# Optimization experiments

Measured on AMD Instinct MI355X. Metric: run time of the kernel, lower is better.

## Reference

```python
import jax, jax.numpy as jnp
import numpy as np

B, S, D, H, E, K = 16, 2048, 768, 3072, 8, 2
CAP_FACTOR = 1.25
LN_EPS = 1e-5


def setup_inputs() -> dict:
    key = jax.random.key(0)
    ks = jax.random.split(key, 6)
    scale = 0.02
    return {
        "x": jax.random.normal(ks[0], (B, S, D), jnp.float32),
        "w_gate": jax.random.normal(ks[1], (D, E), jnp.float32) * scale,  # router (eval: no noise)
        "w1": jax.random.normal(ks[2], (E, D, H), jnp.float32) * scale,
        "b1": jnp.zeros((E, H), jnp.float32),
        "w2": jax.random.normal(ks[3], (E, H, D), jnp.float32) * scale,
        "b2": jnp.zeros((E, D), jnp.float32),
        "ln_w": jnp.ones((D,), jnp.float32),
        "ln_b": jnp.zeros((D,), jnp.float32),
    }


def reference(x, w_gate, w1, b1, w2, b2, ln_w, ln_b):
    b, s, d = x.shape
    n = b * s
    capacity = int(CAP_FACTOR * n * K / E)  # static, matches _compute_capacity
    xf = x.reshape(n, d)

    # NoisyTopKRouter in eval mode: linear gate -> top-k -> softmax over top-k logits
    logits = xf @ w_gate                                   # [N, E]
    top_logits, top_idx = jax.lax.top_k(logits, K)         # [N, K]
    routing = jax.nn.softmax(top_logits, axis=-1)          # [N, K]

    out = jnp.zeros((n, d), x.dtype)
    for e in range(E):
        # per-token weight for expert e (0 if not routed to e)
        w_e = jnp.sum(routing * (top_idx == e), axis=-1)   # [N]
        # capacity dropping: keep the `capacity` highest-weight tokens.
        # Unassigned tokens have weight 0 -> zero contribution, so selecting
        # them as filler is mathematically identical to the torch loop.
        top_w, tok = jax.lax.top_k(w_e, capacity)          # [cap], [cap]
        sel = xf[tok]                                      # gather [cap, D]
        h = jax.nn.gelu(sel @ w1[e] + b1[e], approximate=False)
        y = h @ w2[e] + b2[e]                              # [cap, D]
        out = out.at[tok].add(y * top_w[:, None])          # weighted scatter-add

    out = out.reshape(b, s, d)
    mu = jnp.mean(out, axis=-1, keepdims=True)
    var = jnp.mean(jnp.square(out - mu), axis=-1, keepdims=True)
    return (out - mu) * jax.lax.rsqrt(var + LN_EPS) * ln_w + ln_b
```

## Files before the change

### kernel.cpp

```cpp
#include <hip/hip_runtime.h>
#include <math.h>

#define NTOK 32768
#define DDIM 768
#define HDIM 3072
#define NEXP 8
#define CAP  10240
#define NBLK 128

typedef short short8 __attribute__((ext_vector_type(8)));
typedef float f32x4 __attribute__((ext_vector_type(4)));

__device__ __forceinline__ unsigned short f2bf(float f) {
  unsigned u = __float_as_uint(f);
  u += 0x7FFFu + ((u >> 16) & 1u);
  return (unsigned short)(u >> 16);
}
__device__ __forceinline__ float bf2f(unsigned short h) {
  return __uint_as_float((unsigned)h << 16);
}

__device__ __forceinline__ void gload16(const void* g, void* l) {
  __builtin_amdgcn_global_load_lds(
      (const __attribute__((address_space(1))) void*)g,
      (__attribute__((address_space(3))) void*)l, 16, 0, 0);
}

__device__ __forceinline__ float gelu_fast(float v) {
  float z = v * 0.70710678118654752f;
  float a = fabsf(z);
  float t = 1.0f / (1.0f + 0.3275911f * a);
  float p = t * (0.254829592f +
           t * (-0.284496736f +
           t * (1.421413741f +
           t * (-1.453152027f +
           t * 1.061405429f))));
  float ex = __expf(-a * a);
  float er = 1.0f - p * ex;
  er = copysignf(er, z);
  return 0.5f * v * (1.0f + er);
}

__global__ __launch_bounds__(256) void router_assign(
    const float* __restrict__ x, const float* __restrict__ wg,
    unsigned short* __restrict__ xb,
    unsigned int* __restrict__ pair, float* __restrict__ pw)
{
  __shared__ float wt[NEXP][DDIM];
  int t = threadIdx.x;
  for (int idx = t; idx < NEXP * DDIM; idx += 256) {
    int d = idx >> 3, e = idx & 7;
    wt[e][d] = wg[idx];
  }
  __syncthreads();
  int wave = t >> 6, lane = t & 63;
  int n0 = blockIdx.x * 32 + wave * 8;
  for (int i = 0; i < 8; ++i) {
    int n = n0 + i;
    const float* xr = x + (size_t)n * DDIM;
    unsigned short* xbr = xb + (size_t)n * DDIM;
    float acc[NEXP];
#pragma unroll
    for (int e = 0; e < NEXP; ++e) acc[e] = 0.f;
#pragma unroll
    for (int c = 0; c < 3; ++c) {
      int d = c * 256 + lane * 4;
      float4 xv = *(const float4*)(xr + d);
      ushort4 pk;
      pk.x = f2bf(xv.x); pk.y = f2bf(xv.y); pk.z = f2bf(xv.z); pk.w = f2bf(xv.w);
      *(ushort4*)(xbr + d) = pk;
#pragma unroll
      for (int e = 0; e < NEXP; ++e) {
        float4 wv = *(const float4*)(&wt[e][d]);
        acc[e] += xv.x * wv.x + xv.y * wv.y + xv.z * wv.z + xv.w * wv.w;
      }
    }
#pragma unroll
    for (int e = 0; e < NEXP; ++e) {
      float v = acc[e];
      for (int o = 32; o > 0; o >>= 1) v += __shfl_xor(v, o, 64);
      acc[e] = v;
    }
    if (lane == 0) {
      int e1 = 0; float l1 = acc[0];
#pragma unroll
      for (int e = 1; e < NEXP; ++e) if (acc[e] > l1) { l1 = acc[e]; e1 = e; }
      int e2 = -1; float l2 = -INFINITY;
#pragma unroll
      for (int e = 0; e < NEXP; ++e) if (e != e1 && acc[e] > l2) { l2 = acc[e]; e2 = e; }
      float p1 = 1.f / (1.f + expf(l2 - l1));
      pair[n] = (unsigned)e1 | ((unsigned)e2 << 8);
      pw[n] = p1;
    }
  }
}

__global__ __launch_bounds__(256) void moe_count(
    const unsigned int* __restrict__ pair, int* __restrict__ bcnt)
{
  __shared__ int c8[NEXP];
  int b = blockIdx.x, t = threadIdx.x, lane = t & 63;
  if (t < NEXP) c8[t] = 0;
  __syncthreads();
  unsigned p = pair[b * 256 + t];
  int e1 = p & 255, e2 = (p >> 8) & 255;
#pragma unroll
  for (int e = 0; e < NEXP; ++e) {
    int c = __popcll(__ballot(e1 == e)) + __popcll(__ballot(e2 == e));
    if (lane == 0 && c) atomicAdd(&c8[e], c);
  }
  __syncthreads();
  if (t < NEXP) bcnt[b * NEXP + t] = c8[t];
}

__global__ __launch_bounds__(512) void moe_scan(
    const int* __restrict__ bcnt, int* __restrict__ bbase, int* __restrict__ cnt)
{
  int t = threadIdx.x, w = t >> 6, lane = t & 63;
  if (lane == 0) {
    int run = 0;
    for (int b = 0; b < NBLK; ++b) { bbase[b * NEXP + w] = run; run += bcnt[b * NEXP + w]; }
    cnt[w] = (run < CAP) ? run : CAP;
  }
}

__global__ __launch_bounds__(256) void moe_scatter(
    const unsigned int* __restrict__ pair, const int* __restrict__ bbase,
    int* __restrict__ tokidx, int* __restrict__ slotof)
{
  __shared__ int wcnt[4][NEXP];
  __shared__ int woffs[4][NEXP];
  int b = blockIdx.x, t = threadIdx.x, wave = t >> 6, lane = t & 63;
  int n = b * 256 + t;
  unsigned p = pair[n];
  int e1 = p & 255, e2 = (p >> 8) & 255;
  unsigned long long below = (lane == 63) ? 0x7FFFFFFFFFFFFFFFull
                                          : ((1ull << lane) - 1ull);
  int pre1 = 0, pre2 = 0;
#pragma unroll
  for (int e = 0; e < NEXP; ++e) {
    unsigned long long b1 = __ballot(e1 == e);
    unsigned long long b2 = __ballot(e2 == e);
    if (e1 == e) pre1 = __popcll(b1 & below);
    if (e2 == e) pre2 = __popcll(b1) + __popcll(b2 & below);
    if (lane == 0) wcnt[wave][e] = __popcll(b1) + __popcll(b2);
  }
  __syncthreads();
  if (t < 4 * NEXP) {
    int w = t >> 3, e = t & 7;
    int s = 0;
    for (int w2 = 0; w2 < w; ++w2) s += wcnt[w2][e];
    woffs[w][e] = s;
  }
  __syncthreads();
  int g1 = bbase[b * NEXP + e1] + woffs[wave][e1] + pre1;
  int g2 = bbase[b * NEXP + e2] + woffs[wave][e2] + pre2;
  if (g1 < CAP) { tokidx[e1 * CAP + g1] = n; slotof[2 * n] = e1 * CAP + g1; }
  else slotof[2 * n] = -1;
  if (g2 < CAP) { tokidx[e2 * CAP + g2] = n; slotof[2 * n + 1] = e2 * CAP + g2; }
  else slotof[2 * n + 1] = -1;
}

__global__ __launch_bounds__(256) void transpose_all(
    const float* __restrict__ w1, const float* __restrict__ w2,
    unsigned short* __restrict__ d1, unsigned short* __restrict__ d2)
{
  __shared__ float tile[64][65];
  int bid = blockIdx.x;
  int half = bid / (576 * NEXP);
  int r = bid - half * 576 * NEXP;
  int e = r / 576, rr = r - e * 576;
  const float* src; unsigned short* dst; int R, C, cx, cy;
  if (half == 0) { src = w1; dst = d1; R = DDIM; C = HDIM; cx = rr % 48; cy = rr / 48; }
  else           { src = w2; dst = d2; R = HDIM; C = DDIM; cx = rr % 12; cy = rr / 12; }
  const float* s = src + (size_t)e * R * C;
  unsigned short* d = dst + (size_t)e * R * C;
  int c0 = cx * 64, r0 = cy * 64;
  int tc = threadIdx.x & 63, tg = threadIdx.x >> 6;
#pragma unroll
  for (int q = tg; q < 64; q += 4)
    tile[q][tc] = s[(size_t)(r0 + q) * C + c0 + tc];
  __syncthreads();
#pragma unroll
  for (int q = tg; q < 64; q += 4)
    d[(size_t)(c0 + q) * R + r0 + tc] = f2bf(tile[tc][q]);
}

template<int EPI, int KK, int NN>
__global__ __launch_bounds__(512, 2) void moe_gemm(
    const unsigned short* __restrict__ A,
    const unsigned short* __restrict__ Bt,
    const float* __restrict__ bias,
    const int* __restrict__ cnt,
    const int* __restrict__ tokidx,
    unsigned short* __restrict__ Obuf,
    int mbase, int Mc, int mt)
{
  constexpr int KT = KK / 64;
  constexpr int NI = KT / 2;
  constexpr int GX = NN / 256;

  int nwg = gridDim.x;
  int orig = blockIdx.x;
  int q = nwg >> 3, r = nwg & 7;
  int xcd = orig & 7, loc = orig >> 3;
  int base = (xcd < r) ? xcd * (q + 1) : r * (q + 1) + (xcd - r) * q;
  int wg = base + loc;
  int per_e = GX * mt;
  int e = wg / per_e;
  int rem = wg - e * per_e;
  int by = rem / GX;
  int bx = rem - by * GX;

  int M = cnt[e]; if (M > CAP) M = CAP;
  int ly0 = by * 256;
  int gm0 = mbase + ly0;
  if (gm0 >= M) return;
  int n0 = bx * 256;
  int t = threadIdx.x, wave = t >> 6, lane = t & 63;
  int wr = wave >> 2, wc = wave & 3;
  int lane15 = lane & 15, quad = lane >> 4;

  __shared__ __align__(16) char smem[131072];

  int ci0 = wave * 128 + lane;
  int ci1 = ci0 + 64;
  int r0 = ci0 >> 2, r1 = ci1 >> 2;
  int c0 = (ci0 & 3) ^ ((r0 >> 1) & 3);
  int c1 = (ci1 & 3) ^ ((r1 >> 1) & 3);
  const unsigned short *aB0, *aB1, *bB0, *bB1;
  if (EPI == 0) {
    int g0 = gm0 + r0; if (g0 >= M) g0 = M - 1;
    int g1 = gm0 + r1; if (g1 >= M) g1 = M - 1;
    aB0 = A + (size_t)tokidx[e * CAP + g0] * KK + c0 * 8;
    aB1 = A + (size_t)tokidx[e * CAP + g1] * KK + c1 * 8;
  } else {
    aB0 = A + ((size_t)e * Mc + ly0 + r0) * KK + c0 * 8;
    aB1 = A + ((size_t)e * Mc + ly0 + r1) * KK + c1 * 8;
  }
  bB0 = Bt + ((size_t)e * NN + n0 + r0) * KK + c0 * 8;
  bB1 = Bt + ((size_t)e * NN + n0 + r1) * KK + c1 * 8;

#define STAGE_A(buf, kh, kt_) do { \
    gload16(aB0 + (kt_) * 64 + (kh) * 32, smem + (buf) * 65536 + (kh) * 16384 + wave * 2048); \
    gload16(aB1 + (kt_) * 64 + (kh) * 32, smem + (buf) * 65536 + (kh) * 16384 + wave * 2048 + 1024); \
  } while (0)
#define STAGE_B(buf, kh, kt_) do { \
    gload16(bB0 + (kt_) * 64 + (kh) * 32, smem + (buf) * 65536 + 32768 + (kh) * 16384 + wave * 2048); \
    gload16(bB1 + (kt_) * 64 + (kh) * 32, smem + (buf) * 65536 + 32768 + (kh) * 16384 + wave * 2048 + 1024); \
  } while (0)

  int aoffb[8], boffb[4];
#pragma unroll
  for (int m = 0; m < 8; ++m) {
    int row = wr * 128 + m * 16 + lane15;
    aoffb[m] = row * 64 + ((quad ^ ((row >> 1) & 3)) * 16);
  }
#pragma unroll
  for (int n = 0; n < 4; ++n) {
    int row = wc * 64 + n * 16 + lane15;
    boffb[n] = 32768 + row * 64 + ((quad ^ ((row >> 1) & 3)) * 16);
  }

  f32x4 acc[8][4];
#pragma unroll
  for (int mf = 0; mf < 8; ++mf)
#pragma unroll
    for (int n = 0; n < 4; ++n)
#pragma unroll
      for (int r2 = 0; r2 < 4; ++r2) acc[mf][n][r2] = 0.f;

  short8 af[4], bf[4];

#define BAR()  __builtin_amdgcn_s_barrier()
#define WVM8() asm volatile("s_waitcnt vmcnt(8)" ::: "memory")
#define WVM4() asm volatile("s_waitcnt vmcnt(4)" ::: "memory")
#define WVM0() asm volatile("s_waitcnt vmcnt(0)" ::: "memory")
#define RD_B(buf, ks) do { \
    _Pragma("unroll") \
    for (int n = 0; n < 4; ++n) \
      bf[n] = *(const short8*)(smem + (buf) * 65536 + (ks) * 16384 + boffb[n]); \
  } while (0)
#define RD_A(buf, ks, mh) do { \
    _Pragma("unroll") \
    for (int m = 0; m < 4; ++m) \
      af[m] = *(const short8*)(smem + (buf) * 65536 + (ks) * 16384 + aoffb[(mh) * 4 + m]); \
  } while (0)
#define MM(mh) do { \
    __builtin_amdgcn_s_setprio(1); \
    _Pragma("unroll") \
    for (int m = 0; m < 4; ++m) \
      _Pragma("unroll") \
      for (int n = 0; n < 4; ++n) \
        acc[(mh) * 4 + m][n] = __builtin_amdgcn_mfma_f32_16x16x32_bf16( \
            af[m], bf[n], acc[(mh) * 4 + m][n], 0, 0, 0); \
    __builtin_amdgcn_s_setprio(0); \
  } while (0)

  STAGE_A(0, 0, 0); STAGE_B(0, 0, 0);
  STAGE_A(0, 1, 0); STAGE_B(0, 1, 0);
  STAGE_A(1, 0, 1); STAGE_B(1, 0, 1);
  WVM8();
  BAR();

#pragma unroll 1
  for (int it = 0; it < NI - 1; ++it) {
    int kt = 2 * it;
    RD_B(0, 0); RD_A(0, 0, 0); STAGE_A(1, 1, kt + 1);
    BAR(); MM(0); BAR();
    RD_A(0, 0, 1); STAGE_B(1, 1, kt + 1);
    BAR(); MM(1); WVM8(); BAR();
    RD_B(0, 1); RD_A(0, 1, 0); STAGE_A(0, 0, kt + 2);
    BAR(); MM(0); BAR();
    RD_A(0, 1, 1); STAGE_B(0, 0, kt + 2);
    BAR(); MM(1); WVM8(); BAR();
    RD_B(1, 0); RD_A(1, 0, 0); STAGE_A(0, 1, kt + 2);
    BAR(); MM(0); BAR();
    RD_A(1, 0, 1); STAGE_B(0, 1, kt + 2);
    BAR(); MM(1); WVM8(); BAR();
    RD_B(1, 1); RD_A(1, 1, 0); STAGE_A(1, 0, kt + 3);
    BAR(); MM(0); BAR();
    RD_A(1, 1, 1); STAGE_B(1, 0, kt + 3);
    BAR(); MM(1); WVM8(); BAR();
  }

  {
    constexpr int kt = 2 * (NI - 1);
    RD_B(0, 0); RD_A(0, 0, 0); STAGE_A(1, 1, kt + 1);
    BAR(); MM(0); BAR();
    RD_A(0, 0, 1); STAGE_B(1, 1, kt + 1);
    BAR(); MM(1); WVM8(); BAR();
    RD_B(0, 1); RD_A(0, 1, 0);
    BAR(); MM(0); BAR();
    RD_A(0, 1, 1);
    BAR(); MM(1); WVM4(); BAR();
    RD_B(1, 0); RD_A(1, 0, 0);
    BAR(); MM(0); BAR();
    RD_A(1, 0, 1);
    BAR(); MM(1); WVM0(); BAR();
    RD_B(1, 1); RD_A(1, 1, 0);
    BAR(); MM(0); BAR();
    RD_A(1, 1, 1);
    BAR(); MM(1);
  }

  if (EPI == 0) {
#pragma unroll
    for (int n = 0; n < 4; ++n) {
      int col = n0 + wc * 64 + n * 16 + lane15;
      float bcol = bias[e * NN + col];
#pragma unroll
      for (int mf = 0; mf < 8; ++mf) {
        int rowb = ly0 + wr * 128 + mf * 16 + quad * 4;
#pragma unroll
        for (int r2 = 0; r2 < 4; ++r2) {
          float v = gelu_fast(acc[mf][n][r2] + bcol);
          Obuf[((size_t)e * Mc + rowb + r2) * NN + col] = f2bf(v);
        }
      }
    }
  } else {
    float bc[4];
#pragma unroll
    for (int n = 0; n < 4; ++n)
      bc[n] = bias[e * NN + n0 + wc * 64 + n * 16 + lane15];
#pragma unroll
    for (int mf = 0; mf < 8; ++mf) {
      int gmb = gm0 + wr * 128 + mf * 16 + quad * 4;
#pragma unroll
      for (int r2 = 0; r2 < 4; ++r2) {
        int gm = gmb + r2;
        if (gm < M) {
          unsigned short* yrow = Obuf + ((size_t)e * CAP + gm) * NN;
#pragma unroll
          for (int n = 0; n < 4; ++n) {
            int col = n0 + wc * 64 + n * 16 + lane15;
            yrow[col] = f2bf(acc[mf][n][r2] + bc[n]);
          }
        }
      }
    }
  }
#undef STAGE_A
#undef STAGE_B
#undef BAR
#undef WVM8
#undef WVM4
#undef WVM0
#undef RD_B
#undef RD_A
#undef MM
}

__global__ __launch_bounds__(512) void combine_ln(
    const unsigned short* __restrict__ Y, const int* __restrict__ slotof,
    const float* __restrict__ pw,
    const float* __restrict__ lnw, const float* __restrict__ lnb,
    float* __restrict__ out)
{
  int w = threadIdx.x >> 6, lane = threadIdx.x & 63;
  int n = blockIdx.x * 8 + w;
  int s0 = slotof[2 * n], s1 = slotof[2 * n + 1];
  float p0 = pw[n], p1 = 1.f - p0;
  const unsigned short* y0 = Y + (size_t)(s0 < 0 ? 0 : s0) * DDIM;
  const unsigned short* y1 = Y + (size_t)(s1 < 0 ? 0 : s1) * DDIM;
  if (s0 < 0) p0 = 0.f;
  if (s1 < 0) p1 = 0.f;
  float v[12];
  float s = 0.f, ss = 0.f;
#pragma unroll
  for (int c = 0; c < 3; ++c) {
    int d = c * 256 + lane * 4;
    ushort4 a = *(const ushort4*)(y0 + d);
    ushort4 b = *(const ushort4*)(y1 + d);
    float4 fa = { bf2f(a.x), bf2f(a.y), bf2f(a.z), bf2f(a.w) };
    float4 fb = { bf2f(b.x), bf2f(b.y), bf2f(b.z), bf2f(b.w) };
    v[c * 4 + 0] = p0 * fa.x + p1 * fb.x;
    v[c * 4 + 1] = p0 * fa.y + p1 * fb.y;
    v[c * 4 + 2] = p0 * fa.z + p1 * fb.z;
    v[c * 4 + 3] = p0 * fa.w + p1 * fb.w;
#pragma unroll
    for (int j = 0; j < 4; ++j) { s += v[c * 4 + j]; ss += v[c * 4 + j] * v[c * 4 + j]; }
  }
  for (int o = 32; o > 0; o >>= 1) { s += __shfl_xor(s, o, 64); ss += __shfl_xor(ss, o, 64); }
  float mu = s * (1.f / DDIM);
  float var = ss * (1.f / DDIM) - mu * mu;
  float rs = rsqrtf(var + 1e-5f);
  float* row = out + (size_t)n * DDIM;
#pragma unroll
  for (int c = 0; c < 3; ++c) {
    int d = c * 256 + lane * 4;
    float4 lw = *(const float4*)(lnw + d);
    float4 lb = *(const float4*)(lnb + d);
    float4 o;
    o.x = (v[c * 4 + 0] - mu) * rs * lw.x + lb.x;
    o.y = (v[c * 4 + 1] - mu) * rs * lw.y + lb.y;
    o.z = (v[c * 4 + 2] - mu) * rs * lw.z + lb.z;
    o.w = (v[c * 4 + 3] - mu) * rs * lw.w + lb.w;
    *(float4*)(row + d) = o;
  }
}

__global__ void sentinel_kernel(float* __restrict__ out, int n) {
  int i = blockIdx.x * 256 + threadIdx.x;
  if (i < n) out[i] = 12345.0f;
}

extern "C" void kernel_launch(void* const* d_in, const int* in_sizes, int n_in,
                              void* d_out, int out_size, void* d_ws, size_t ws_size,
                              hipStream_t stream)
{
  const float* x   = (const float*)d_in[0];
  const float* wg  = (const float*)d_in[1];
  const float* w1  = (const float*)d_in[2];
  const float* b1  = (const float*)d_in[3];
  const float* w2  = (const float*)d_in[4];
  const float* b2  = (const float*)d_in[5];
  const float* lnw = (const float*)d_in[6];
  const float* lnb = (const float*)d_in[7];
  float* out = (float*)d_out;

  char* ws = (char*)d_ws;
  size_t off = 0;
  auto take = [&](size_t bytes) {
    char* p = ws + off; off += (bytes + 255) & ~(size_t)255; return p;
  };
  unsigned short* xb   = (unsigned short*)take((size_t)NTOK * DDIM * 2);
  unsigned short* w1bt = (unsigned short*)take((size_t)NEXP * DDIM * HDIM * 2);
  unsigned short* w2bt = (unsigned short*)take((size_t)NEXP * DDIM * HDIM * 2);
  int*   tokidx = (int*)take((size_t)NEXP * CAP * 4);
  unsigned int* pair = (unsigned int*)take((size_t)NTOK * 4);
  float* pw   = (float*)take((size_t)NTOK * 4);
  int*   slotof = (int*)take((size_t)NTOK * 2 * 4);
  int*   cnt  = (int*)take(256);
  int*   bcnt  = (int*)take((size_t)NBLK * NEXP * 4);
  int*   bbase = (int*)take((size_t)NBLK * NEXP * 4);
  unsigned short* Ybuf = (unsigned short*)take((size_t)NEXP * CAP * DDIM * 2);

  size_t avail = (ws_size > off) ? (ws_size - off) : 0;
  long long cand = (long long)(avail / ((size_t)NEXP * HDIM * 2));
  int Mc = (int)((cand / 256) * 256);
  if (Mc > CAP) Mc = CAP;
  if (Mc < 256) {
    sentinel_kernel<<<(NTOK * DDIM + 255) / 256, 256, 0, stream>>>(out, NTOK * DDIM);
    return;
  }
  unsigned short* Hbuf = (unsigned short*)take((size_t)NEXP * Mc * HDIM * 2);

  router_assign<<<NTOK / 32, 256, 0, stream>>>(x, wg, xb, pair, pw);
  transpose_all<<<576 * NEXP * 2, 256, 0, stream>>>(w1, w2, w1bt, w2bt);
  moe_count<<<NBLK, 256, 0, stream>>>(pair, bcnt);
  moe_scan<<<1, 512, 0, stream>>>(bcnt, bbase, cnt);
  moe_scatter<<<NBLK, 256, 0, stream>>>(pair, bbase, tokidx, slotof);

  for (int mbase = 0; mbase < CAP; mbase += Mc) {
    int rows = CAP - mbase; if (rows > Mc) rows = Mc;
    int mt = rows / 256;
    moe_gemm<0, DDIM, HDIM><<<(HDIM / 256) * mt * NEXP, 512, 0, stream>>>(
        xb, w1bt, b1, cnt, tokidx, Hbuf, mbase, Mc, mt);
    moe_gemm<1, HDIM, DDIM><<<(DDIM / 256) * mt * NEXP, 512, 0, stream>>>(
        Hbuf, w2bt, b2, cnt, tokidx, Ybuf, mbase, Mc, mt);
  }

  combine_ln<<<NTOK / 8, 512, 0, stream>>>(Ybuf, slotof, pw, lnw, lnb, out);
}
```

Baseline: 1.450 ms.

## Make MoE GEMM persistent with cross-tile prefetch and fuse routing scatter into router

The expert GEMM kernel becomes persistent: a grid of at most 256 workgroups walks a contiguous range of tiles, and the next tile's first K-slices are prefetched into LDS during the last K-steps of the current tile, hiding the pipeline prologue. Separately, the count/scan/scatter kernels are removed and slot assignment is done inside the router kernel with per-block atomics on expert counters, which requires a memset of the counters. The atomic ordering makes slot assignment nondeterministic, so which tokens get dropped at capacity can differ from the reference ordering. Fewer workgroups may also reduce latency hiding.

```diff
diff --git a/kernel.cpp b/kernel.cpp
--- a/kernel.cpp
+++ b/kernel.cpp
@@ -6,7 +6,6 @@
 #define HDIM 3072
 #define NEXP 8
 #define CAP  10240
-#define NBLK 128
 
 typedef short short8 __attribute__((ext_vector_type(8)));
 typedef float f32x4 __attribute__((ext_vector_type(4)));
@@ -44,9 +43,12 @@
 __global__ __launch_bounds__(256) void router_assign(
     const float* __restrict__ x, const float* __restrict__ wg,
     unsigned short* __restrict__ xb,
-    unsigned int* __restrict__ pair, float* __restrict__ pw)
+    float* __restrict__ pw, int* __restrict__ cnt,
+    int* __restrict__ tokidx, int* __restrict__ slotof)
 {
   __shared__ float wt[NEXP][DDIM];
+  __shared__ unsigned spair[32];
+  __shared__ int sbase[NEXP];
   int t = threadIdx.x;
   for (int idx = t; idx < NEXP * DDIM; idx += 256) {
     int d = idx >> 3, e = idx & 7;
@@ -89,76 +91,40 @@
 #pragma unroll
       for (int e = 0; e < NEXP; ++e) if (e != e1 && acc[e] > l2) { l2 = acc[e]; e2 = e; }
       float p1 = 1.f / (1.f + expf(l2 - l1));
-      pair[n] = (unsigned)e1 | ((unsigned)e2 << 8);
+      spair[wave * 8 + i] = (unsigned)e1 | ((unsigned)e2 << 8);
       pw[n] = p1;
     }
   }
-}
-
-__global__ __launch_bounds__(256) void moe_count(
-    const unsigned int* __restrict__ pair, int* __restrict__ bcnt)
-{
-  __shared__ int c8[NEXP];
-  int b = blockIdx.x, t = threadIdx.x, lane = t & 63;
-  if (t < NEXP) c8[t] = 0;
   __syncthreads();
-  unsigned p = pair[b * 256 + t];
-  int e1 = p & 255, e2 = (p >> 8) & 255;
-#pragma unroll
-  for (int e = 0; e < NEXP; ++e) {
-    int c = __popcll(__ballot(e1 == e)) + __popcll(__ballot(e2 == e));
-    if (lane == 0 && c) atomicAdd(&c8[e], c);
+  int e1 = 0, e2 = 0, r1 = 0, r2 = 0;
+  if (t < 32) {
+    unsigned mep = spair[t];
+    e1 = mep & 255; e2 = (mep >> 8) & 255;
+    for (int j = 0; j < t; ++j) {
+      unsigned pj = spair[j];
+      int f1 = pj & 255, f2 = (pj >> 8) & 255;
+      r1 += (f1 == e1) + (f2 == e1);
+      r2 += (f1 == e2) + (f2 == e2);
+    }
+  }
+  if (t < NEXP) {
+    int tot = 0;
+    for (int j = 0; j < 32; ++j) {
+      unsigned pj = spair[j];
+      tot += ((pj & 255) == (unsigned)t) + (((pj >> 8) & 255) == (unsigned)t);
+    }
+    sbase[t] = atomicAdd(&cnt[t], tot);
   }
   __syncthreads();
-  if (t < NEXP) bcnt[b * NEXP + t] = c8[t];
-}
-
-__global__ __launch_bounds__(512) void moe_scan(
-    const int* __restrict__ bcnt, int* __restrict__ bbase, int* __restrict__ cnt)
-{
-  int t = threadIdx.x, w = t >> 6, lane = t & 63;
-  if (lane == 0) {
-    int run = 0;
-    for (int b = 0; b < NBLK; ++b) { bbase[b * NEXP + w] = run; run += bcnt[b * NEXP + w]; }
-    cnt[w] = (run < CAP) ? run : CAP;
-  }
-}
-
-__global__ __launch_bounds__(256) void moe_scatter(
-    const unsigned int* __restrict__ pair, const int* __restrict__ bbase,
-    int* __restrict__ tokidx, int* __restrict__ slotof)
-{
-  __shared__ int wcnt[4][NEXP];
-  __shared__ int woffs[4][NEXP];
-  int b = blockIdx.x, t = threadIdx.x, wave = t >> 6, lane = t & 63;
-  int n = b * 256 + t;
-  unsigned p = pair[n];
-  int e1 = p & 255, e2 = (p >> 8) & 255;
-  unsigned long long below = (lane == 63) ? 0x7FFFFFFFFFFFFFFFull
-                                          : ((1ull << lane) - 1ull);
-  int pre1 = 0, pre2 = 0;
-#pragma unroll
-  for (int e = 0; e < NEXP; ++e) {
-    unsigned long long b1 = __ballot(e1 == e);
-    unsigned long long b2 = __ballot(e2 == e);
-    if (e1 == e) pre1 = __popcll(b1 & below);
-    if (e2 == e) pre2 = __popcll(b1) + __popcll(b2 & below);
-    if (lane == 0) wcnt[wave][e] = __popcll(b1) + __popcll(b2);
-  }
-  __syncthreads();
-  if (t < 4 * NEXP) {
-    int w = t >> 3, e = t & 7;
-    int s = 0;
-    for (int w2 = 0; w2 < w; ++w2) s += wcnt[w2][e];
-    woffs[w][e] = s;
-  }
-  __syncthreads();
-  int g1 = bbase[b * NEXP + e1] + woffs[wave][e1] + pre1;
-  int g2 = bbase[b * NEXP + e2] + woffs[wave][e2] + pre2;
-  if (g1 < CAP) { tokidx[e1 * CAP + g1] = n; slotof[2 * n] = e1 * CAP + g1; }
-  else slotof[2 * n] = -1;
-  if (g2 < CAP) { tokidx[e2 * CAP + g2] = n; slotof[2 * n + 1] = e2 * CAP + g2; }
-  else slotof[2 * n + 1] = -1;
+  if (t < 32) {
+    int n = blockIdx.x * 32 + t;
+    int g1 = sbase[e1] + r1;
+    int g2 = sbase[e2] + r2;
+    if (g1 < CAP) { tokidx[e1 * CAP + g1] = n; slotof[2 * n] = e1 * CAP + g1; }
+    else slotof[2 * n] = -1;
+    if (g2 < CAP) { tokidx[e2 * CAP + g2] = n; slotof[2 * n + 1] = e2 * CAP + g2; }
+    else slotof[2 * n + 1] = -1;
+  }
 }
 
 __global__ __launch_bounds__(256) void transpose_all(
@@ -200,23 +166,6 @@
   constexpr int NI = KT / 2;
   constexpr int GX = NN / 256;
 
-  int nwg = gridDim.x;
-  int orig = blockIdx.x;
-  int q = nwg >> 3, r = nwg & 7;
-  int xcd = orig & 7, loc = orig >> 3;
-  int base = (xcd < r) ? xcd * (q + 1) : r * (q + 1) + (xcd - r) * q;
-  int wg = base + loc;
-  int per_e = GX * mt;
-  int e = wg / per_e;
-  int rem = wg - e * per_e;
-  int by = rem / GX;
-  int bx = rem - by * GX;
-
-  int M = cnt[e]; if (M > CAP) M = CAP;
-  int ly0 = by * 256;
-  int gm0 = mbase + ly0;
-  if (gm0 >= M) return;
-  int n0 = bx * 256;
   int t = threadIdx.x, wave = t >> 6, lane = t & 63;
   int wr = wave >> 2, wc = wave & 3;
   int lane15 = lane & 15, quad = lane >> 4;
@@ -228,27 +177,46 @@
   int r0 = ci0 >> 2, r1 = ci1 >> 2;
   int c0 = (ci0 & 3) ^ ((r0 >> 1) & 3);
   int c1 = (ci1 & 3) ^ ((r1 >> 1) & 3);
-  const unsigned short *aB0, *aB1, *bB0, *bB1;
-  if (EPI == 0) {
-    int g0 = gm0 + r0; if (g0 >= M) g0 = M - 1;
-    int g1 = gm0 + r1; if (g1 >= M) g1 = M - 1;
-    aB0 = A + (size_t)tokidx[e * CAP + g0] * KK + c0 * 8;
-    aB1 = A + (size_t)tokidx[e * CAP + g1] * KK + c1 * 8;
-  } else {
-    aB0 = A + ((size_t)e * Mc + ly0 + r0) * KK + c0 * 8;
-    aB1 = A + ((size_t)e * Mc + ly0 + r1) * KK + c1 * 8;
-  }
-  bB0 = Bt + ((size_t)e * NN + n0 + r0) * KK + c0 * 8;
-  bB1 = Bt + ((size_t)e * NN + n0 + r1) * KK + c1 * 8;
-
-#define STAGE_A(buf, kh, kt_) do { \
-    gload16(aB0 + (kt_) * 64 + (kh) * 32, smem + (buf) * 65536 + (kh) * 16384 + wave * 2048); \
-    gload16(aB1 + (kt_) * 64 + (kh) * 32, smem + (buf) * 65536 + (kh) * 16384 + wave * 2048 + 1024); \
-  } while (0)
-#define STAGE_B(buf, kh, kt_) do { \
-    gload16(bB0 + (kt_) * 64 + (kh) * 32, smem + (buf) * 65536 + 32768 + (kh) * 16384 + wave * 2048); \
-    gload16(bB1 + (kt_) * 64 + (kh) * 32, smem + (buf) * 65536 + 32768 + (kh) * 16384 + wave * 2048 + 1024); \
-  } while (0)
+
+  int L = NEXP * mt * GX;
+  int per_e = mt * GX;
+  int g = gridDim.x;
+  int p = (blockIdx.x & 7) * (g >> 3) + (blockIdx.x >> 3);
+  int q = L / g, rr_ = L % g;
+  int s_ = p * q + (p < rr_ ? p : rr_);
+  int endi = s_ + q + (p < rr_ ? 1 : 0);
+
+  const unsigned short *cA0, *cA1, *cB0, *cB1;
+  int cE, cLy, cGm, cN0, cM;
+
+  auto mktile = [&](int tau, const unsigned short*& A0, const unsigned short*& A1,
+                    const unsigned short*& B0, const unsigned short*& B1,
+                    int& tE, int& tLy, int& tGm, int& tN0, int& tM) -> bool {
+    int e = tau / per_e; int rem = tau - e * per_e;
+    int by = rem / GX; int bx = rem - by * GX;
+    int M = cnt[e]; if (M > CAP) M = CAP;
+    int ly0 = by * 256, gm0 = mbase + ly0, n0 = bx * 256;
+    tE = e; tLy = ly0; tGm = gm0; tN0 = n0; tM = M;
+    if (gm0 >= M) return false;
+    if (EPI == 0) {
+      int g0 = gm0 + r0; if (g0 >= M) g0 = M - 1;
+      int g1 = gm0 + r1; if (g1 >= M) g1 = M - 1;
+      A0 = A + (size_t)tokidx[e * CAP + g0] * KK + c0 * 8;
+      A1 = A + (size_t)tokidx[e * CAP + g1] * KK + c1 * 8;
+    } else {
+      A0 = A + ((size_t)e * Mc + ly0 + r0) * KK + c0 * 8;
+      A1 = A + ((size_t)e * Mc + ly0 + r1) * KK + c1 * 8;
+    }
+    B0 = Bt + ((size_t)e * NN + n0 + r0) * KK + c0 * 8;
+    B1 = Bt + ((size_t)e * NN + n0 + r1) * KK + c1 * 8;
+    return true;
+  };
+
+  int ci = s_;
+  bool have = false;
+  for (; ci < endi; ++ci)
+    if (mktile(ci, cA0, cA1, cB0, cB1, cE, cLy, cGm, cN0, cM)) { have = true; break; }
+  if (!have) return;
 
   int aoffb[8], boffb[4];
 #pragma unroll
@@ -262,20 +230,14 @@
     boffb[n] = 32768 + row * 64 + ((quad ^ ((row >> 1) & 3)) * 16);
   }
 
-  f32x4 acc[8][4];
-#pragma unroll
-  for (int mf = 0; mf < 8; ++mf)
-#pragma unroll
-    for (int n = 0; n < 4; ++n)
-#pragma unroll
-      for (int r2 = 0; r2 < 4; ++r2) acc[mf][n][r2] = 0.f;
-
   short8 af[4], bf[4];
 
+#define STG(P0, P1, dst_off, src_off) do { \
+    gload16((P0) + (src_off), smem + (dst_off) + wave * 2048); \
+    gload16((P1) + (src_off), smem + (dst_off) + wave * 2048 + 1024); \
+  } while (0)
 #define BAR()  __builtin_amdgcn_s_barrier()
 #define WVM8() asm volatile("s_waitcnt vmcnt(8)" ::: "memory")
-#define WVM4() asm volatile("s_waitcnt vmcnt(4)" ::: "memory")
-#define WVM0() asm volatile("s_waitcnt vmcnt(0)" ::: "memory")
 #define RD_B(buf, ks) do { \
     _Pragma("unroll") \
     for (int n = 0; n < 4; ++n) \
@@ -297,96 +259,115 @@
     __builtin_amdgcn_s_setprio(0); \
   } while (0)
 
-  STAGE_A(0, 0, 0); STAGE_B(0, 0, 0);
-  STAGE_A(0, 1, 0); STAGE_B(0, 1, 0);
-  STAGE_A(1, 0, 1); STAGE_B(1, 0, 1);
+  STG(cA0, cA1, 0,             0);   STG(cB0, cB1, 32768,         0);
+  STG(cA0, cA1, 16384,        32);   STG(cB0, cB1, 49152,        32);
+  STG(cA0, cA1, 65536,        64);   STG(cB0, cB1, 98304,        64);
   WVM8();
   BAR();
 
+  for (;;) {
+    int nj = ci + 1;
+    const unsigned short *nA0 = cA0, *nA1 = cA1, *nB0 = cB0, *nB1 = cB1;
+    int nE, nLy, nGm, nN0, nM;
+    bool hn = false;
+    for (; nj < endi; ++nj)
+      if (mktile(nj, nA0, nA1, nB0, nB1, nE, nLy, nGm, nN0, nM)) { hn = true; break; }
+
+    f32x4 acc[8][4];
+#pragma unroll
+    for (int mf = 0; mf < 8; ++mf)
+#pragma unroll
+      for (int n = 0; n < 4; ++n)
+#pragma unroll
+        for (int r2 = 0; r2 < 4; ++r2) acc[mf][n][r2] = 0.f;
+
 #pragma unroll 1
-  for (int it = 0; it < NI - 1; ++it) {
-    int kt = 2 * it;
-    RD_B(0, 0); RD_A(0, 0, 0); STAGE_A(1, 1, kt + 1);
-    BAR(); MM(0); BAR();
-    RD_A(0, 0, 1); STAGE_B(1, 1, kt + 1);
-    BAR(); MM(1); WVM8(); BAR();
-    RD_B(0, 1); RD_A(0, 1, 0); STAGE_A(0, 0, kt + 2);
-    BAR(); MM(0); BAR();
-    RD_A(0, 1, 1); STAGE_B(0, 0, kt + 2);
-    BAR(); MM(1); WVM8(); BAR();
-    RD_B(1, 0); RD_A(1, 0, 0); STAGE_A(0, 1, kt + 2);
-    BAR(); MM(0); BAR();
-    RD_A(1, 0, 1); STAGE_B(0, 1, kt + 2);
-    BAR(); MM(1); WVM8(); BAR();
-    RD_B(1, 1); RD_A(1, 1, 0); STAGE_A(1, 0, kt + 3);
-    BAR(); MM(0); BAR();
-    RD_A(1, 1, 1); STAGE_B(1, 0, kt + 3);
-    BAR(); MM(1); WVM8(); BAR();
-  }
-
-  {
-    constexpr int kt = 2 * (NI - 1);
-    RD_B(0, 0); RD_A(0, 0, 0); STAGE_A(1, 1, kt + 1);
-    BAR(); MM(0); BAR();
-    RD_A(0, 0, 1); STAGE_B(1, 1, kt + 1);
-    BAR(); MM(1); WVM8(); BAR();
-    RD_B(0, 1); RD_A(0, 1, 0);
-    BAR(); MM(0); BAR();
-    RD_A(0, 1, 1);
-    BAR(); MM(1); WVM4(); BAR();
-    RD_B(1, 0); RD_A(1, 0, 0);
-    BAR(); MM(0); BAR();
-    RD_A(1, 0, 1);
-    BAR(); MM(1); WVM0(); BAR();
-    RD_B(1, 1); RD_A(1, 1, 0);
-    BAR(); MM(0); BAR();
-    RD_A(1, 1, 1);
-    BAR(); MM(1);
-  }
-
-  if (EPI == 0) {
-#pragma unroll
-    for (int n = 0; n < 4; ++n) {
-      int col = n0 + wc * 64 + n * 16 + lane15;
-      float bcol = bias[e * NN + col];
-#pragma unroll
-      for (int mf = 0; mf < 8; ++mf) {
-        int rowb = ly0 + wr * 128 + mf * 16 + quad * 4;
-#pragma unroll
-        for (int r2 = 0; r2 < 4; ++r2) {
-          float v = gelu_fast(acc[mf][n][r2] + bcol);
-          Obuf[((size_t)e * Mc + rowb + r2) * NN + col] = f2bf(v);
-        }
-      }
-    }
-  } else {
-    float bc[4];
-#pragma unroll
-    for (int n = 0; n < 4; ++n)
-      bc[n] = bias[e * NN + n0 + wc * 64 + n * 16 + lane15];
-#pragma unroll
-    for (int mf = 0; mf < 8; ++mf) {
-      int gmb = gm0 + wr * 128 + mf * 16 + quad * 4;
-#pragma unroll
-      for (int r2 = 0; r2 < 4; ++r2) {
-        int gm = gmb + r2;
-        if (gm < M) {
-          unsigned short* yrow = Obuf + ((size_t)e * CAP + gm) * NN;
-#pragma unroll
-          for (int n = 0; n < 4; ++n) {
-            int col = n0 + wc * 64 + n * 16 + lane15;
-            yrow[col] = f2bf(acc[mf][n][r2] + bc[n]);
+    for (int it = 0; it < NI - 1; ++it) {
+      int kt = 2 * it;
+      RD_B(0, 0); RD_A(0, 0, 0); STG(cA0, cA1, 81920, (kt + 1) * 64 + 32);
+      BAR(); MM(0); BAR();
+      RD_A(0, 0, 1); STG(cB0, cB1, 114688, (kt + 1) * 64 + 32);
+      BAR(); MM(1); WVM8(); BAR();
+      RD_B(0, 1); RD_A(0, 1, 0); STG(cA0, cA1, 0, (kt + 2) * 64);
+      BAR(); MM(0); BAR();
+      RD_A(0, 1, 1); STG(cB0, cB1, 32768, (kt + 2) * 64);
+      BAR(); MM(1); WVM8(); BAR();
+      RD_B(1, 0); RD_A(1, 0, 0); STG(cA0, cA1, 16384, (kt + 2) * 64 + 32);
+      BAR(); MM(0); BAR();
+      RD_A(1, 0, 1); STG(cB0, cB1, 49152, (kt + 2) * 64 + 32);
+      BAR(); MM(1); WVM8(); BAR();
+      RD_B(1, 1); RD_A(1, 1, 0); STG(cA0, cA1, 65536, (kt + 3) * 64);
+      BAR(); MM(0); BAR();
+      RD_A(1, 1, 1); STG(cB0, cB1, 98304, (kt + 3) * 64);
+      BAR(); MM(1); WVM8(); BAR();
+    }
+
+    {
+      constexpr int kt = KT - 2;
+      RD_B(0, 0); RD_A(0, 0, 0); STG(cA0, cA1, 81920, (kt + 1) * 64 + 32);
+      BAR(); MM(0); BAR();
+      RD_A(0, 0, 1); STG(cB0, cB1, 114688, (kt + 1) * 64 + 32);
+      BAR(); MM(1); WVM8(); BAR();
+      RD_B(0, 1); RD_A(0, 1, 0); STG(nA0, nA1, 0, 0);
+      BAR(); MM(0); BAR();
+      RD_A(0, 1, 1); STG(nB0, nB1, 32768, 0);
+      BAR(); MM(1); WVM8(); BAR();
+      RD_B(1, 0); RD_A(1, 0, 0); STG(nA0, nA1, 16384, 32);
+      BAR(); MM(0); BAR();
+      RD_A(1, 0, 1); STG(nB0, nB1, 49152, 32);
+      BAR(); MM(1); WVM8(); BAR();
+      RD_B(1, 1); RD_A(1, 1, 0); STG(nA0, nA1, 65536, 64);
+      BAR(); MM(0); BAR();
+      RD_A(1, 1, 1); STG(nB0, nB1, 98304, 64);
+      BAR(); MM(1); WVM8(); BAR();
+    }
+
+    if (EPI == 0) {
+#pragma unroll
+      for (int n = 0; n < 4; ++n) {
+        int col = cN0 + wc * 64 + n * 16 + lane15;
+        float bcol = bias[cE * NN + col];
+#pragma unroll
+        for (int mf = 0; mf < 8; ++mf) {
+          int rowb = cLy + wr * 128 + mf * 16 + quad * 4;
+#pragma unroll
+          for (int r2 = 0; r2 < 4; ++r2) {
+            float v = gelu_fast(acc[mf][n][r2] + bcol);
+            Obuf[((size_t)cE * Mc + rowb + r2) * NN + col] = f2bf(v);
           }
         }
       }
-    }
-  }
-#undef STAGE_A
-#undef STAGE_B
+    } else {
+      float bc[4];
+#pragma unroll
+      for (int n = 0; n < 4; ++n)
+        bc[n] = bias[cE * NN + cN0 + wc * 64 + n * 16 + lane15];
+#pragma unroll
+      for (int mf = 0; mf < 8; ++mf) {
+        int gmb = cGm + wr * 128 + mf * 16 + quad * 4;
+#pragma unroll
+        for (int r2 = 0; r2 < 4; ++r2) {
+          int gm = gmb + r2;
+          if (gm < cM) {
+            unsigned short* yrow = Obuf + ((size_t)cE * CAP + gm) * NN;
+#pragma unroll
+            for (int n = 0; n < 4; ++n) {
+              int col = cN0 + wc * 64 + n * 16 + lane15;
+              yrow[col] = f2bf(acc[mf][n][r2] + bc[n]);
+            }
+          }
+        }
+      }
+    }
+
+    if (!hn) break;
+    cA0 = nA0; cA1 = nA1; cB0 = nB0; cB1 = nB1;
+    cE = nE; cLy = nLy; cGm = nGm; cN0 = nN0; cM = nM;
+    ci = nj;
+  }
+#undef STG
 #undef BAR
 #undef WVM8
-#undef WVM4
-#undef WVM0
 #undef RD_B
 #undef RD_A
 #undef MM
@@ -469,12 +450,9 @@
   unsigned short* w1bt = (unsigned short*)take((size_t)NEXP * DDIM * HDIM * 2);
   unsigned short* w2bt = (unsigned short*)take((size_t)NEXP * DDIM * HDIM * 2);
   int*   tokidx = (int*)take((size_t)NEXP * CAP * 4);
-  unsigned int* pair = (unsigned int*)take((size_t)NTOK * 4);
   float* pw   = (float*)take((size_t)NTOK * 4);
   int*   slotof = (int*)take((size_t)NTOK * 2 * 4);
   int*   cnt  = (int*)take(256);
-  int*   bcnt  = (int*)take((size_t)NBLK * NEXP * 4);
-  int*   bbase = (int*)take((size_t)NBLK * NEXP * 4);
   unsigned short* Ybuf = (unsigned short*)take((size_t)NEXP * CAP * DDIM * 2);
 
   size_t avail = (ws_size > off) ? (ws_size - off) : 0;
@@ -487,19 +465,25 @@
   }
   unsigned short* Hbuf = (unsigned short*)take((size_t)NEXP * Mc * HDIM * 2);
 
-  router_assign<<<NTOK / 32, 256, 0, stream>>>(x, wg, xb, pair, pw);
+  hipMemsetAsync(cnt, 0, NEXP * sizeof(int), stream);
+  router_assign<<<NTOK / 32, 256, 0, stream>>>(x, wg, xb, pw, cnt, tokidx, slotof);
   transpose_all<<<576 * NEXP * 2, 256, 0, stream>>>(w1, w2, w1bt, w2bt);
-  moe_count<<<NBLK, 256, 0, stream>>>(pair, bcnt);
-  moe_scan<<<1, 512, 0, stream>>>(bcnt, bbase, cnt);
-  moe_scatter<<<NBLK, 256, 0, stream>>>(pair, bbase, tokidx, slotof);
 
   for (int mbase = 0; mbase < CAP; mbase += Mc) {
     int rows = CAP - mbase; if (rows > Mc) rows = Mc;
     int mt = rows / 256;
-    moe_gemm<0, DDIM, HDIM><<<(HDIM / 256) * mt * NEXP, 512, 0, stream>>>(
-        xb, w1bt, b1, cnt, tokidx, Hbuf, mbase, Mc, mt);
-    moe_gemm<1, HDIM, DDIM><<<(DDIM / 256) * mt * NEXP, 512, 0, stream>>>(
-        Hbuf, w2bt, b2, cnt, tokidx, Ybuf, mbase, Mc, mt);
+    {
+      int L = NEXP * mt * (HDIM / 256);
+      int g = L / 2; if (g > 256) g = 256; g &= ~7; if (g < 8) g = 8;
+      moe_gemm<0, DDIM, HDIM><<<g, 512, 0, stream>>>(
+          xb, w1bt, b1, cnt, tokidx, Hbuf, mbase, Mc, mt);
+    }
+    {
+      int L = NEXP * mt * (DDIM / 256);
+      int g = L / 2; if (g > 256) g = 256; g &= ~7; if (g < 8) g = 8;
+      moe_gemm<1, HDIM, DDIM><<<g, 512, 0, stream>>>(
+          Hbuf, w2bt, b2, cnt, tokidx, Ybuf, mbase, Mc, mt);
+    }
   }
 
   combine_ln<<<NTOK / 8, 512, 0, stream>>>(Ybuf, slotof, pw, lnw, lnb, out);
```

After: 1.738 ms. +19.9%, slower.
